# Kernel optimization log

Hardware: AMD Instinct MI355X
Metric: run time of the kernel (lower is better)

## Reference

```python
import jax, jax.numpy as jnp
import numpy as np

N, NH, G, SEG, RATIO = 500000, 128, 10000, 25, 2
P = G * SEG            # 250000 pos samples
PN = P * RATIO         # 500000 neg samples


def setup_inputs() -> dict:
    key = jax.random.key(0)
    k1, k2, k3, k4, k5, k6 = jax.random.split(key, 6)
    return {
        "embedding": jax.random.normal(k1, (N, NH), jnp.float32),
        "embedding_": jax.random.normal(k2, (N, NH), jnp.float32),
        "grid_sizes": jnp.full((G,), SEG, dtype=jnp.int64 if jax.config.jax_enable_x64 else jnp.int32),
        "pos_samples": jax.random.randint(k3, (P,), 0, N),
        "neg_samples": jax.random.randint(k4, (PN,), 0, N),
        "Wi": jax.random.normal(k5, (NH, NH), jnp.float32) * (1.0 / np.sqrt(NH)),
        "bi": jnp.zeros((NH,), jnp.float32),
        "Wk": jax.random.normal(k6, (NH, NH), jnp.float32) * (1.0 / np.sqrt(NH)),  # Bilinear weight [1,nh,nh] squeezed
        "bk": jnp.zeros((1,), jnp.float32),
    }


def reference(embedding, embedding_, grid_sizes, pos_samples, neg_samples, Wi, bi, Wk, bk):
    Pl = pos_samples.shape[0]
    Gl = grid_sizes.shape[0]
    ratio = neg_samples.shape[0] // Pl  # static int

    # segment ids: grid index repeated grid_sizes[i] times (sum == P)
    seg_ids = jnp.repeat(jnp.arange(Gl), grid_sizes, total_repeat_length=Pl)

    # f_i on embedding_ , gather pos, segment-mean per grid
    emb_ = embedding_ @ Wi.T + bi                      # [N, nh]
    pos_e_ = emb_[pos_samples]                         # [P, nh]
    seg_sum = jax.ops.segment_sum(pos_e_, seg_ids, num_segments=Gl)
    grid_embed = seg_sum / grid_sizes[:, None].astype(seg_sum.dtype)  # [G, nh]

    # f_i on embedding, gather pos/neg samples
    emb = embedding @ Wi.T + bi
    pos_embed = emb[pos_samples]                       # [P, nh]
    neg_embed = emb[neg_samples]                       # [P*ratio, nh]

    # broadcast grid embedding back to per-sample rows
    pos_grid = grid_embed[seg_ids]                     # [P, nh]
    neg_seg_ids = jnp.repeat(jnp.arange(Gl), grid_sizes * ratio,
                             total_repeat_length=Pl * ratio)
    neg_grid = grid_embed[neg_seg_ids]                 # [P*ratio, nh]

    # bilinear score: x1 W x2 + b (out features = 1, squeezed)
    pos_logits = jnp.einsum('nd,de,ne->n', pos_embed, Wk, pos_grid) + bk[0]
    neg_logits = jnp.einsum('nd,de,ne->n', neg_embed, Wk, neg_grid) + bk[0]
    return jnp.concatenate((pos_logits, neg_logits))
```

## Files before the change

kernel.cpp:

```cpp
#include <hip/hip_runtime.h>

#define NH 128

__global__ void scan_kernel(const int* __restrict__ gs, int* __restrict__ c, int G) {
    __shared__ int part[1024];
    int t = threadIdx.x;
    int chunk = (G + 1023) >> 10;
    int b = t * chunk;
    int e = min(b + chunk, G);
    int s = 0;
    for (int i = b; i < e; ++i) s += gs[i];
    part[t] = s;
    __syncthreads();
    for (int off = 1; off < 1024; off <<= 1) {
        int val = (t >= off) ? part[t - off] : 0;
        __syncthreads();
        part[t] += val;
        __syncthreads();
    }
    int excl = (t == 0) ? 0 : part[t - 1];
    for (int i = b; i < e; ++i) { c[i] = excl; excl += gs[i]; }
    if (t == 1023) c[G] = part[1023];
}

__global__ void matA_kernel(const float* __restrict__ Wk, const float* __restrict__ Wi,
                            const float* __restrict__ bi,
                            float* __restrict__ A, float* __restrict__ u) {
    int tid = blockIdx.x * blockDim.x + threadIdx.x;
    int e = tid >> 7, d = tid & (NH - 1);
    float acc = 0.f;
    for (int f = 0; f < NH; ++f) acc += Wk[e * NH + f] * Wi[f * NH + d];
    A[e * NH + d] = acc;
    if (tid < NH) {
        float s = 0.f;
        for (int f = 0; f < NH; ++f) s += Wk[tid * NH + f] * bi[f];
        u[tid] = s;
    }
}

__global__ void matB_kernel(const float* __restrict__ Wi, const float* __restrict__ bi,
                            const float* __restrict__ bk,
                            const float* __restrict__ A, const float* __restrict__ u,
                            float* __restrict__ Bt, float* __restrict__ v,
                            float* __restrict__ w, float* __restrict__ s0) {
    int tid = blockIdx.x * blockDim.x + threadIdx.x;
    int i = tid & (NH - 1);
    int j = tid >> 7;
    float acc = 0.f;
    for (int e = 0; e < NH; ++e) acc += Wi[e * NH + i] * A[e * NH + j];
    Bt[j * NH + i] = acc;
    if (tid < NH) {
        float s = 0.f;
        for (int e = 0; e < NH; ++e) s += Wi[e * NH + tid] * u[e];
        v[tid] = s;
    } else if (tid < 2 * NH) {
        int jj = tid - NH;
        float s = 0.f;
        for (int e = 0; e < NH; ++e) s += bi[e] * A[e * NH + jj];
        w[jj] = s;
    }
    if (tid == 0) {
        float s = 0.f;
        for (int e = 0; e < NH; ++e) s += bi[e] * u[e];
        s0[0] = s + bk[0];
    }
}

#define SEGS_PER_BLOCK 8
__global__ void seg_kernel(const float* __restrict__ emb_, const int* __restrict__ pos,
                           const int* __restrict__ c,
                           const float* __restrict__ Bt, const float* __restrict__ v,
                           const float* __restrict__ w, const float* __restrict__ s0,
                           float* __restrict__ Q, float* __restrict__ C2, int G) {
    __shared__ float m[SEGS_PER_BLOCK][NH];
    __shared__ float red[SEGS_PER_BLOCK][2];
    int d = threadIdx.x;
    int g0 = blockIdx.x * SEGS_PER_BLOCK;
    int ns = min(SEGS_PER_BLOCK, G - g0);

    for (int s = 0; s < SEGS_PER_BLOCK; ++s) {
        float acc = 0.f;
        if (s < ns) {
            int b = c[g0 + s], e = c[g0 + s + 1];
            for (int i = b; i < e; ++i)
                acc += emb_[(size_t)pos[i] * NH + d];
            acc /= (float)(e - b);
        }
        m[s][d] = acc;
    }
    __syncthreads();

    float q[SEGS_PER_BLOCK];
#pragma unroll
    for (int s = 0; s < SEGS_PER_BLOCK; ++s) q[s] = 0.f;
    for (int f = 0; f < NH; ++f) {
        float bt = Bt[f * NH + d];
#pragma unroll
        for (int s = 0; s < SEGS_PER_BLOCK; ++s) q[s] += bt * m[s][f];
    }
    float vd = v[d], wd = w[d], s00 = s0[0];
    for (int s = 0; s < ns; ++s)
        Q[(size_t)(g0 + s) * NH + d] = q[s] + vd;

    int lane = d & 63, wv = d >> 6;
    for (int s = 0; s < SEGS_PER_BLOCK; ++s) {
        float t = wd * m[s][d];
        for (int off = 32; off; off >>= 1) t += __shfl_xor(t, off);
        if (lane == 0) red[s][wv] = t;
    }
    __syncthreads();
    if (d < SEGS_PER_BLOCK && d < ns) C2[g0 + d] = red[d][0] + red[d][1] + s00;
}

__global__ void logits_kernel(const float* __restrict__ emb, const int* __restrict__ pos,
                              const int* __restrict__ neg, const int* __restrict__ c,
                              const float* __restrict__ Q, const float* __restrict__ C2,
                              float* __restrict__ out, int P, int ratio) {
    __shared__ float q[NH];
    int g = blockIdx.x;
    int t = threadIdx.x;
    if (t < NH) q[t] = Q[(size_t)g * NH + t];
    __syncthreads();
    float c2 = C2[g];
    int pb = c[g], pe = c[g + 1];
    int wv = t >> 6, lane = t & 63;
    float q0 = q[2 * lane], q1 = q[2 * lane + 1];

    for (int i = pb + wv; i < pe; i += 4) {
        const float2 a = ((const float2*)(emb + (size_t)pos[i] * NH))[lane];
        float val = a.x * q0 + a.y * q1;
        for (int off = 32; off; off >>= 1) val += __shfl_xor(val, off);
        if (lane == 0) out[i] = val + c2;
    }
    int nb = pb * ratio, ne = pe * ratio;
    for (int j = nb + wv; j < ne; j += 4) {
        const float2 a = ((const float2*)(emb + (size_t)neg[j] * NH))[lane];
        float val = a.x * q0 + a.y * q1;
        for (int off = 32; off; off >>= 1) val += __shfl_xor(val, off);
        if (lane == 0) out[P + j] = val + c2;
    }
}

extern "C" void kernel_launch(void* const* d_in, const int* in_sizes, int n_in,
                              void* d_out, int out_size, void* d_ws, size_t ws_size,
                              hipStream_t stream) {
    const float* embedding  = (const float*)d_in[0];
    const float* embedding_ = (const float*)d_in[1];
    const int*   grid_sizes = (const int*)d_in[2];
    const int*   pos        = (const int*)d_in[3];
    const int*   neg        = (const int*)d_in[4];
    const float* Wi         = (const float*)d_in[5];
    const float* bi         = (const float*)d_in[6];
    const float* Wk         = (const float*)d_in[7];
    const float* bk         = (const float*)d_in[8];

    int G = in_sizes[2];
    int P = in_sizes[3];
    int PN = in_sizes[4];
    int ratio = PN / P;

    char* ws = (char*)d_ws;
    size_t off = 0;
    auto alloc = [&](size_t bytes) {
        void* p = ws + off;
        off += (bytes + 255) & ~(size_t)255;
        return p;
    };
    int*   c   = (int*)  alloc((size_t)(G + 1) * sizeof(int));
    float* A   = (float*)alloc(NH * NH * sizeof(float));
    float* u   = (float*)alloc(NH * sizeof(float));
    float* Bt  = (float*)alloc(NH * NH * sizeof(float));
    float* v   = (float*)alloc(NH * sizeof(float));
    float* w   = (float*)alloc(NH * sizeof(float));
    float* s0  = (float*)alloc(sizeof(float));
    float* Q   = (float*)alloc((size_t)G * NH * sizeof(float));
    float* C2  = (float*)alloc((size_t)G * sizeof(float));
    (void)ws_size; (void)n_in; (void)out_size;

    hipLaunchKernelGGL(scan_kernel, dim3(1), dim3(1024), 0, stream, grid_sizes, c, G);
    hipLaunchKernelGGL(matA_kernel, dim3((NH * NH) / 256), dim3(256), 0, stream,
                       Wk, Wi, bi, A, u);
    hipLaunchKernelGGL(matB_kernel, dim3((NH * NH) / 256), dim3(256), 0, stream,
                       Wi, bi, bk, A, u, Bt, v, w, s0);
    hipLaunchKernelGGL(seg_kernel, dim3((G + SEGS_PER_BLOCK - 1) / SEGS_PER_BLOCK), dim3(NH), 0, stream,
                       embedding_, pos, c, Bt, v, w, s0, Q, C2, G);
    hipLaunchKernelGGL(logits_kernel, dim3(G), dim3(256), 0, stream,
                       embedding, pos, neg, c, Q, C2, (float*)d_out, P, ratio);
}
```

Before: 653.5 us.

## Split segment mean into its own kernel and vectorize gathers with float4

Segment-mean gathering moves into a separate kernel with one block per segment: eight 32-lane groups each read whole rows as float4 and are then reduced through shared memory. Previously one 128-thread block handled 8 segments serially. The Q projection now reads the precomputed means from a new workspace buffer. The logits kernel stages pos and neg indices in shared memory and uses 32-lane float4 row loads, so one block processes more rows at once. The goals are more memory-level parallelism for the random-row gathers and more rows in flight. The cost is an extra launch and an extra global round-trip for the means.

```diff
diff --git a/kernel.cpp b/kernel.cpp
--- a/kernel.cpp
+++ b/kernel.cpp
@@ -66,78 +66,104 @@
     }
 }
 
-#define SEGS_PER_BLOCK 8
-__global__ void seg_kernel(const float* __restrict__ emb_, const int* __restrict__ pos,
-                           const int* __restrict__ c,
-                           const float* __restrict__ Bt, const float* __restrict__ v,
-                           const float* __restrict__ w, const float* __restrict__ s0,
-                           float* __restrict__ Q, float* __restrict__ C2, int G) {
-    __shared__ float m[SEGS_PER_BLOCK][NH];
-    __shared__ float red[SEGS_PER_BLOCK][2];
+__global__ void seg_mean_kernel(const float* __restrict__ emb_, const int* __restrict__ pos,
+                                const int* __restrict__ c, float* __restrict__ M, int G) {
+    __shared__ float smf[8 * NH];
+    int g = blockIdx.x;
+    int t = threadIdx.x;
+    int lane = t & 31, slot = t >> 5;
+    int b = c[g], e = c[g + 1];
+    float4 acc = make_float4(0.f, 0.f, 0.f, 0.f);
+    for (int r = b + slot; r < e; r += 8) {
+        int row = pos[r];
+        const float4 a = ((const float4*)(emb_ + (size_t)row * NH))[lane];
+        acc.x += a.x; acc.y += a.y; acc.z += a.z; acc.w += a.w;
+    }
+    ((float4*)(smf + slot * NH))[lane] = acc;
+    __syncthreads();
+    if (t < NH) {
+        float s = 0.f;
+#pragma unroll
+        for (int s2 = 0; s2 < 8; ++s2) s += smf[s2 * NH + t];
+        float cnt = (float)max(e - b, 1);
+        M[(size_t)g * NH + t] = s / cnt;
+    }
+}
+
+#define SPB 8
+__global__ void q_kernel(const float* __restrict__ M, const float* __restrict__ Bt,
+                         const float* __restrict__ v, const float* __restrict__ w,
+                         const float* __restrict__ s0,
+                         float* __restrict__ Q, float* __restrict__ C2, int G) {
+    __shared__ float m[SPB][NH];
+    __shared__ float red[SPB][2];
     int d = threadIdx.x;
-    int g0 = blockIdx.x * SEGS_PER_BLOCK;
-    int ns = min(SEGS_PER_BLOCK, G - g0);
-
-    for (int s = 0; s < SEGS_PER_BLOCK; ++s) {
-        float acc = 0.f;
-        if (s < ns) {
-            int b = c[g0 + s], e = c[g0 + s + 1];
-            for (int i = b; i < e; ++i)
-                acc += emb_[(size_t)pos[i] * NH + d];
-            acc /= (float)(e - b);
-        }
-        m[s][d] = acc;
-    }
-    __syncthreads();
-
-    float q[SEGS_PER_BLOCK];
-#pragma unroll
-    for (int s = 0; s < SEGS_PER_BLOCK; ++s) q[s] = 0.f;
+    int g0 = blockIdx.x * SPB;
+    int ns = min(SPB, G - g0);
+    for (int s = 0; s < SPB; ++s)
+        m[s][d] = (s < ns) ? M[(size_t)(g0 + s) * NH + d] : 0.f;
+    __syncthreads();
+
+    float q[SPB];
+#pragma unroll
+    for (int s = 0; s < SPB; ++s) q[s] = 0.f;
     for (int f = 0; f < NH; ++f) {
         float bt = Bt[f * NH + d];
 #pragma unroll
-        for (int s = 0; s < SEGS_PER_BLOCK; ++s) q[s] += bt * m[s][f];
+        for (int s = 0; s < SPB; ++s) q[s] += bt * m[s][f];
     }
     float vd = v[d], wd = w[d], s00 = s0[0];
     for (int s = 0; s < ns; ++s)
         Q[(size_t)(g0 + s) * NH + d] = q[s] + vd;
 
     int lane = d & 63, wv = d >> 6;
-    for (int s = 0; s < SEGS_PER_BLOCK; ++s) {
-        float t = wd * m[s][d];
-        for (int off = 32; off; off >>= 1) t += __shfl_xor(t, off);
-        if (lane == 0) red[s][wv] = t;
-    }
-    __syncthreads();
-    if (d < SEGS_PER_BLOCK && d < ns) C2[g0 + d] = red[d][0] + red[d][1] + s00;
+    for (int s = 0; s < SPB; ++s) {
+        float tval = wd * m[s][d];
+        for (int off = 32; off; off >>= 1) tval += __shfl_xor(tval, off);
+        if (lane == 0) red[s][wv] = tval;
+    }
+    __syncthreads();
+    if (d < SPB && d < ns) C2[g0 + d] = red[d][0] + red[d][1] + s00;
 }
 
 __global__ void logits_kernel(const float* __restrict__ emb, const int* __restrict__ pos,
                               const int* __restrict__ neg, const int* __restrict__ c,
                               const float* __restrict__ Q, const float* __restrict__ C2,
                               float* __restrict__ out, int P, int ratio) {
-    __shared__ float q[NH];
+    __shared__ float qs[NH];
+    __shared__ int idx[512];
     int g = blockIdx.x;
     int t = threadIdx.x;
-    if (t < NH) q[t] = Q[(size_t)g * NH + t];
-    __syncthreads();
+    if (t < NH) qs[t] = Q[(size_t)g * NH + t];
+    int pb = c[g], pe = c[g + 1];
+    int np = pe - pb;
+    int nb = pb * ratio;
+    int tot = np + np * ratio;
+    int lane = t & 31, slot = t >> 5;
+    __syncthreads();
+    float4 qr = ((const float4*)qs)[lane];
     float c2 = C2[g];
-    int pb = c[g], pe = c[g + 1];
-    int wv = t >> 6, lane = t & 63;
-    float q0 = q[2 * lane], q1 = q[2 * lane + 1];
-
-    for (int i = pb + wv; i < pe; i += 4) {
-        const float2 a = ((const float2*)(emb + (size_t)pos[i] * NH))[lane];
-        float val = a.x * q0 + a.y * q1;
-        for (int off = 32; off; off >>= 1) val += __shfl_xor(val, off);
-        if (lane == 0) out[i] = val + c2;
-    }
-    int nb = pb * ratio, ne = pe * ratio;
-    for (int j = nb + wv; j < ne; j += 4) {
-        const float2 a = ((const float2*)(emb + (size_t)neg[j] * NH))[lane];
-        float val = a.x * q0 + a.y * q1;
-        for (int off = 32; off; off >>= 1) val += __shfl_xor(val, off);
-        if (lane == 0) out[P + j] = val + c2;
+
+    for (int k0 = 0; k0 < tot; k0 += 512) {
+        int kend = min(tot - k0, 512);
+        __syncthreads();
+        for (int k = t; k < kend; k += 256) {
+            int kk = k0 + k;
+            idx[k] = (kk < np) ? pos[pb + kk] : neg[nb + kk - np];
+        }
+        __syncthreads();
+        for (int k = slot; k < kend; k += 8) {
+            int kk = k0 + k;
+            int row = idx[k];
+            const float4 a = ((const float4*)(emb + (size_t)row * NH))[lane];
+            float val = a.x * qr.x + a.y * qr.y + a.z * qr.z + a.w * qr.w;
+#pragma unroll
+            for (int off = 16; off; off >>= 1) val += __shfl_xor(val, off, 32);
+            if (lane == 0) {
+                int o = (kk < np) ? (pb + kk) : (P + nb + kk - np);
+                out[o] = val + c2;
+            }
+        }
     }
 }
 
@@ -175,6 +201,7 @@
     float* s0  = (float*)alloc(sizeof(float));
     float* Q   = (float*)alloc((size_t)G * NH * sizeof(float));
     float* C2  = (float*)alloc((size_t)G * sizeof(float));
+    float* M   = (float*)alloc((size_t)G * NH * sizeof(float));
     (void)ws_size; (void)n_in; (void)out_size;
 
     hipLaunchKernelGGL(scan_kernel, dim3(1), dim3(1024), 0, stream, grid_sizes, c, G);
@@ -182,8 +209,10 @@
                        Wk, Wi, bi, A, u);
     hipLaunchKernelGGL(matB_kernel, dim3((NH * NH) / 256), dim3(256), 0, stream,
                        Wi, bi, bk, A, u, Bt, v, w, s0);
-    hipLaunchKernelGGL(seg_kernel, dim3((G + SEGS_PER_BLOCK - 1) / SEGS_PER_BLOCK), dim3(NH), 0, stream,
-                       embedding_, pos, c, Bt, v, w, s0, Q, C2, G);
+    hipLaunchKernelGGL(seg_mean_kernel, dim3(G), dim3(256), 0, stream,
+                       embedding_, pos, c, M, G);
+    hipLaunchKernelGGL(q_kernel, dim3((G + SPB - 1) / SPB), dim3(NH), 0, stream,
+                       M, Bt, v, w, s0, Q, C2, G);
     hipLaunchKernelGGL(logits_kernel, dim3(G), dim3(256), 0, stream,
                        embedding, pos, neg, c, Q, C2, (float*)d_out, P, ratio);
 }
```

After: 541.6 us. 17.1% less time.
